# Optimization experiments

Hardware: AMD Instinct MI355X
Metric: run time of the kernel (lower is better)

The kernel has to match this reference:

```python
import jax, jax.numpy as jnp
import numpy as np
from jax import lax

B, T, C, H, W = 1, 6, 64, 128, 128
DG, K = 16, 9          # deformable groups, 3x3 kernel positions
CG = C // DG
MRM = 10.0             # max_residue_magnitude


def _conv3(x, w, b):
    y = lax.conv_general_dilated(x, w, (1, 1), 'SAME',
                                 dimension_numbers=('NCHW', 'OIHW', 'NCHW'))
    return y + b[None, :, None, None]


def _leaky(x):
    return jnp.where(x >= 0, x, 0.1 * x)


def _bilinear(img, py, px):
    # img [N,Cc,h,w]; py/px [N,*S] unnormalized pixel coords; zero padding outside.
    N, Cc, h, w = img.shape
    S = py.shape[1:]
    py = py.reshape(N, -1)
    px = px.reshape(N, -1)
    y0 = jnp.floor(py); x0 = jnp.floor(px)
    fy = py - y0; fx = px - x0
    y0 = y0.astype(jnp.int32); x0 = x0.astype(jnp.int32)
    imf = img.reshape(N, Cc, h * w)

    def corner(yi, xi, wt):
        valid = (yi >= 0) & (yi < h) & (xi >= 0) & (xi < w)
        idx = jnp.clip(yi, 0, h - 1) * w + jnp.clip(xi, 0, w - 1)
        v = jax.vmap(lambda im, ix: im[:, ix])(imf, idx)  # [N,Cc,M]
        return v * (wt * valid)[:, None, :]

    out = (corner(y0, x0, (1 - fy) * (1 - fx))
           + corner(y0, x0 + 1, (1 - fy) * fx)
           + corner(y0 + 1, x0, fy * (1 - fx))
           + corner(y0 + 1, x0 + 1, fy * fx))
    return out.reshape(N, Cc, *S)


def _flow_warp(x, flow):
    # flow [N,2,H,W]: channel 0 = x-displacement, channel 1 = y-displacement
    gy = jnp.arange(H, dtype=jnp.float32)
    gx = jnp.arange(W, dtype=jnp.float32)
    py = gy[None, :, None] + flow[:, 1]
    px = gx[None, None, :] + flow[:, 0]
    return _bilinear(x, py, px)


def _mod_deform_conv(x, offset, mask, w, b):
    # offset [N, 2*DG*K, H, W] interleaved (y,x) per (group, kernel pos); mask [N, DG*K, H, W]
    N = x.shape[0]
    off = offset.reshape(N, DG, K, 2, H, W)
    kh = (jnp.arange(K) // 3).astype(jnp.float32)
    kw = (jnp.arange(K) % 3).astype(jnp.float32)
    gy = jnp.arange(H, dtype=jnp.float32)
    gx = jnp.arange(W, dtype=jnp.float32)
    # stride 1, padding 1, dilation 1, 3x3 kernel
    py = gy[None, None, None, :, None] - 1.0 + kh[None, None, :, None, None] + off[:, :, :, 0]
    px = gx[None, None, None, None, :] - 1.0 + kw[None, None, :, None, None] + off[:, :, :, 1]
    xg = x.reshape(N, DG, CG, H, W).reshape(N * DG, CG, H, W)
    s = _bilinear(xg, py.reshape(N * DG, K, H, W), px.reshape(N * DG, K, H, W))
    s = s.reshape(N, DG, CG, K, H, W) * mask.reshape(N, DG, 1, K, H, W)
    wr = w.reshape(C, DG, CG, K)
    return jnp.einsum('ngckhw,ogck->nohw', s, wr) + b[None, :, None, None]


def setup_inputs() -> dict:
    key = jax.random.key(0)
    ks = jax.random.split(key, 10)
    rn = lambda k, s, sc: jax.random.normal(k, s, jnp.float32) * sc
    cin = 2 * C + 2  # (1 + n_frames//2)*C + n_frames
    return {
        'x': rn(ks[0], (B, T, C, H, W), 1.0),
        'flows_backward': rn(ks[1], (B, T - 1, 2, H, W), 2.0),
        'flows_forward': rn(ks[2], (B, T - 1, 2, H, W), 2.0),
        'cw1': rn(ks[3], (C, cin, 3, 3), 1.0 / np.sqrt(cin * 9)),
        'cb1': jnp.zeros((C,), jnp.float32),
        'cw2': rn(ks[4], (C, C, 3, 3), 1.0 / np.sqrt(C * 9)),
        'cb2': jnp.zeros((C,), jnp.float32),
        'cw3': rn(ks[5], (C, C, 3, 3), 1.0 / np.sqrt(C * 9)),
        'cb3': jnp.zeros((C,), jnp.float32),
        # original zero-inits the last conv; use small random so offsets/masks are nontrivial
        'cw4': rn(ks[6], (3 * K * DG, C, 3, 3), 0.01),
        'cb4': jnp.zeros((3 * K * DG,), jnp.float32),
        'dcn_w': rn(ks[7], (C, C, 3, 3), 1.0 / np.sqrt(C * 9)),
        'dcn_b': jnp.zeros((C,), jnp.float32),
    }


def reference(x, flows_backward, flows_forward, cw1, cb1, cw2, cb2, cw3, cb3,
              cw4, cb4, dcn_w, dcn_b):
    # Batch all backward-pass frame pairs (i=T-1..1) and forward-pass pairs (i=0..T-2)
    # into one effective batch of B*2*(T-1) independent DCN calls.
    xi = jnp.concatenate([x[:, 1:], x[:, :-1]], axis=1)      # source frames
    cur = jnp.concatenate([x[:, :-1], x[:, 1:]], axis=1)     # target (current) frames
    fl = jnp.concatenate([flows_backward, flows_forward], axis=1)
    N = B * 2 * (T - 1)
    xi = xi.reshape(N, C, H, W)
    cur = cur.reshape(N, C, H, W)
    fl = fl.reshape(N, 2, H, W)

    warped = _flow_warp(xi, fl)
    inp = jnp.concatenate([warped, cur, fl], axis=1)          # [N, 2C+2, H, W]
    h1 = _leaky(_conv3(inp, cw1, cb1))
    h2 = _leaky(_conv3(h1, cw2, cb2))
    h3 = _leaky(_conv3(h2, cw3, cb3))
    out = _conv3(h3, cw4, cb4)                                # [N, 3*9*DG, H, W]
    o1, o2, m = jnp.split(out, 3, axis=1)
    offset = MRM * jnp.tanh(jnp.concatenate([o1, o2], axis=1))
    # flow.flip(1).repeat -> interleaved (fy, fx) added to every (group, kernel pos)
    offset = offset + jnp.tile(fl[:, ::-1], (1, DG * K, 1, 1))
    mask = jax.nn.sigmoid(m)

    feat = _mod_deform_conv(xi, offset, mask, dcn_w, dcn_b)   # [N, C, H, W]
    feat = feat.reshape(B, 2, T - 1, C, H, W)
    zeros = jnp.zeros((B, 1, C, H, W), feat.dtype)
    x_backward = jnp.concatenate([feat[:, 0], zeros], axis=1)  # [B, T, C, H, W]
    x_forward = jnp.concatenate([zeros, feat[:, 1]], axis=1)   # [B, T, C, H, W]
    return x_backward, x_forward
```

## Files before the change

### kernel.cpp

```cpp
#include <hip/hip_runtime.h>
#include <math.h>

#define NP   10
#define C_   64
#define H_   128
#define W_   128
#define HW   (H_*W_)
#define MRM_ 10.0f

#define A_OFF   0u
#define SV_OFF  41472u
#define OMB_OFF 66048u
#define LDS_TOT 81408

#define W1T_N 82944
#define W2T_N 36864
#define W4_N  294912
#define DWT_N 49152

typedef __bf16 bf16x8 __attribute__((ext_vector_type(8)));
typedef float  f32x16 __attribute__((ext_vector_type(16)));

__device__ __forceinline__ f32x16 mfma32(bf16x8 a, bf16x8 b, f32x16 c) {
    return __builtin_amdgcn_mfma_f32_32x32x16_bf16(a, b, c, 0, 0, 0);
}

__device__ __forceinline__ ushort bfrn(float f) {
    uint u = __builtin_bit_cast(uint, f);
    u += 0x7FFFu + ((u >> 16) & 1u);
    return (ushort)(u >> 16);
}
__device__ __forceinline__ float blo(uint u) { return __builtin_bit_cast(float, u << 16); }
__device__ __forceinline__ float bhi(uint u) { return __builtin_bit_cast(float, u & 0xFFFF0000u); }
__device__ __forceinline__ float fast_tanh(float x) {
    float e = __expf(2.f * x);
    return 1.f - 2.f / (e + 1.f);
}

__device__ __forceinline__ const float* xi_base(const float* x, int n) {
    int f = (n < 5) ? (n + 1) : (n - 5);
    return x + (size_t)f * C_ * HW;
}
__device__ __forceinline__ const float* cur_base(const float* x, int n) {
    int f = (n < 5) ? n : (n - 4);
    return x + (size_t)f * C_ * HW;
}
__device__ __forceinline__ const float* fl_base(const float* fb, const float* ff, int n) {
    return (n < 5) ? (fb + (size_t)n * 2 * HW) : (ff + (size_t)(n - 5) * 2 * HW);
}

struct Bil { int i00, i01, i10, i11; float m00, m01, m10, m11; };
__device__ __forceinline__ Bil bil(float py, float px) {
    float y0f = floorf(py), x0f = floorf(px);
    int iy0 = (int)y0f, ix0 = (int)x0f;
    float ay = py - y0f, ax = px - x0f;
    bool v0y = (unsigned)iy0 < (unsigned)H_;
    bool v1y = (unsigned)(iy0 + 1) < (unsigned)H_;
    bool v0x = (unsigned)ix0 < (unsigned)W_;
    bool v1x = (unsigned)(ix0 + 1) < (unsigned)W_;
    int cy0 = min(max(iy0, 0), H_ - 1), cy1 = min(max(iy0 + 1, 0), H_ - 1);
    int cx0 = min(max(ix0, 0), W_ - 1), cx1 = min(max(ix0 + 1, 0), W_ - 1);
    Bil r;
    r.m00 = (1.f - ay) * (1.f - ax) * (float)(v0y && v0x);
    r.m01 = (1.f - ay) * ax         * (float)(v0y && v1x);
    r.m10 = ay * (1.f - ax)         * (float)(v1y && v0x);
    r.m11 = ay * ax                 * (float)(v1y && v1x);
    r.i00 = cy0 * W_ + cx0; r.i01 = cy0 * W_ + cx1;
    r.i10 = cy1 * W_ + cx0; r.i11 = cy1 * W_ + cx1;
    return r;
}

__global__ __launch_bounds__(256) void k_prep(
        const float* __restrict__ cw1, const float* __restrict__ cw2,
        const float* __restrict__ cw3, const float* __restrict__ cw4,
        const float* __restrict__ cb4, const float* __restrict__ dw,
        ushort* __restrict__ w1t, ushort* __restrict__ w2t,
        ushort* __restrict__ w3t, ushort* __restrict__ w4t,
        ushort* __restrict__ dwtb, float* __restrict__ pb4) {
    int id = blockIdx.x * 256 + threadIdx.x;
    if (id < W1T_N) {
        int blk = id >> 9, e = id & 511;
        int c = blk / 18, r = blk % 18; int t = r >> 1, nf = r & 1;
        int l = e >> 3, j = e & 7;
        int ci = c * 16 + (l >> 5) * 8 + j;
        int oc = nf * 32 + (l & 31);
        w1t[id] = (ci < 130) ? bfrn(cw1[((size_t)oc * 130 + ci) * 9 + t]) : (ushort)0;
        return;
    }
    id -= W1T_N;
    if (id < W2T_N) {
        int blk = id >> 9, e = id & 511;
        int c = blk / 18, r = blk % 18; int t = r >> 1, nf = r & 1;
        int l = e >> 3, j = e & 7;
        int ci = c * 16 + (l >> 5) * 8 + j;
        int oc = nf * 32 + (l & 31);
        w2t[id] = bfrn(cw2[((size_t)oc * 64 + ci) * 9 + t]);
        return;
    }
    id -= W2T_N;
    if (id < W2T_N) {
        int blk = id >> 9, e = id & 511;
        int c = blk / 18, r = blk % 18; int t = r >> 1, nf = r & 1;
        int l = e >> 3, j = e & 7;
        int ci = c * 16 + (l >> 5) * 8 + j;
        int oc = nf * 32 + (l & 31);
        w3t[id] = bfrn(cw3[((size_t)oc * 64 + ci) * 9 + t]);
        return;
    }
    id -= W2T_N;
    if (id < W4_N) {
        int blk = id >> 9, e = id & 511;
        int c = blk / 144, r = blk - c * 144;
        int t = r >> 4, g = r & 15;
        int l = e >> 3, j = e & 7;
        int nn = l & 31, kh = l >> 5;
        int ci = c * 16 + kh * 8 + j;
        int ch = (nn < 18) ? g * 18 + nn : (nn < 27 ? 288 + g * 9 + (nn - 18) : -1);
        float v = (ch >= 0) ? cw4[((size_t)ch * 64 + ci) * 9 + t] : 0.f;
        w4t[id] = bfrn(v);
        return;
    }
    id -= W4_N;
    if (id < DWT_N) {
        int blk = id >> 9, e = id & 511;
        int g = blk / 6, r = blk - g * 6;
        int kst = r >> 1, nf = r & 1;
        int l = e >> 3, j = e & 7;
        int kk = kst * 16 + (l >> 5) * 8 + j;
        int oc = nf * 32 + (l & 31);
        float v = (kk < 36) ? dw[((size_t)oc * 64 + g * 4 + (kk & 3)) * 9 + (kk >> 2)] : 0.f;
        dwtb[id] = bfrn(v);
        return;
    }
    id -= DWT_N;
    if (id < 512) {
        int g = id >> 5, nn = id & 31;
        int ch = (nn < 18) ? g * 18 + nn : (nn < 27 ? 288 + g * 9 + (nn - 18) : -1);
        pb4[id] = (ch >= 0) ? cb4[ch] : 0.f;
    }
}

__global__ __launch_bounds__(256) void k_warp(
        const float* __restrict__ x, const float* __restrict__ fb,
        const float* __restrict__ ff, ushort* __restrict__ warped) {
    int gid = blockIdx.x * 256 + threadIdx.x;
    int n = gid / HW, pos = gid % HW;
    int y = pos / W_, xx = pos % W_;
    const float* fl = fl_base(fb, ff, n);
    float fx = fl[pos], fy = fl[HW + pos];
    Bil b = bil((float)y + fy, (float)xx + fx);
    const float* xb = xi_base(x, n);
    ushort* wout = warped + (size_t)n * C_ * HW + pos;
    for (int c = 0; c < C_; ++c) {
        const float* p = xb + c * HW;
        wout[c * HW] = bfrn(b.m00 * p[b.i00] + b.m01 * p[b.i01]
                          + b.m10 * p[b.i10] + b.m11 * p[b.i11]);
    }
}

__global__ __launch_bounds__(256) void k_xt(
        const float* __restrict__ x, ushort* __restrict__ xt) {
    int gid = blockIdx.x * 256 + threadIdx.x;
    int f = gid / HW, pos = gid % HW;
    const float* src = x + (size_t)f * C_ * HW + pos;
    ushort* dst = xt + ((size_t)f * HW + pos) * 64;
    #pragma unroll
    for (int c8 = 0; c8 < 8; ++c8) {
        uint4 v;
        ushort h0 = bfrn(src[(c8 * 8 + 0) * HW]);
        ushort h1 = bfrn(src[(c8 * 8 + 1) * HW]);
        ushort h2 = bfrn(src[(c8 * 8 + 2) * HW]);
        ushort h3 = bfrn(src[(c8 * 8 + 3) * HW]);
        ushort h4 = bfrn(src[(c8 * 8 + 4) * HW]);
        ushort h5 = bfrn(src[(c8 * 8 + 5) * HW]);
        ushort h6 = bfrn(src[(c8 * 8 + 6) * HW]);
        ushort h7 = bfrn(src[(c8 * 8 + 7) * HW]);
        v.x = (uint)h0 | ((uint)h1 << 16);
        v.y = (uint)h2 | ((uint)h3 << 16);
        v.z = (uint)h4 | ((uint)h5 << 16);
        v.w = (uint)h6 | ((uint)h7 << 16);
        *(uint4*)(dst + c8 * 8) = v;
    }
}

template<int NCHUNK, int SRC>
__global__ __launch_bounds__(256, 3) void k_convm(
        const ushort* __restrict__ inb, const float* __restrict__ x,
        const float* __restrict__ fb, const float* __restrict__ ff,
        const ushort* __restrict__ wt, const float* __restrict__ bias,
        ushort* __restrict__ outp) {
    __shared__ __align__(16) char ldsb[41472];
    int tid = threadIdx.x;
    int lane = tid & 63, w = tid >> 6;
    int id = (blockIdx.x & 7) * 80 + (blockIdx.x >> 3);
    int bx = id & 7, by = (id >> 3) & 7, n = id >> 6;
    int col = lane & 31, khalf = lane >> 5;

    const float* flp = fl_base(fb, ff, n);
    const float* curp = cur_base(x, n);

    f32x16 acc[2][2];
    #pragma unroll
    for (int a = 0; a < 2; ++a)
        #pragma unroll
        for (int b = 0; b < 2; ++b)
            #pragma unroll
            for (int r = 0; r < 16; ++r) acc[a][b][r] = 0.f;

    int xb2 = col & 15;
    int rb0 = 4 * w + ((col >> 4) & 1);
    const int NPASS = (NCHUNK + 3) / 4;

    #pragma unroll
    for (int p = 0; p < NPASS; ++p) {
        const int c0 = 4 * p;
        const int cN = (NCHUNK - c0 >= 4) ? 4 : (NCHUNK - c0);
        __syncthreads();
        for (int cc = 0; cc < cN; ++cc) {
            int chunk = c0 + cc;
            int cbase = chunk * 16 + w * 4;
            for (int v = 0; v < 6; ++v) {
                int cell = v * 64 + lane;
                if (cell < 324) {
                    int cy = cell / 18, cx = cell - cy * 18;
                    int gy = by * 16 + cy - 1, gx = bx * 16 + cx - 1;
                    bool ok = ((unsigned)gy < 128u) && ((unsigned)gx < 128u);
                    int pos = gy * W_ + gx;
                    uint2 hv; hv.x = hv.y = 0;
                    if (SRC == 1 || chunk < 4) {
                        const ushort* sp = inb + ((size_t)n * 64 + cbase) * HW + pos;
                        ushort h0 = ok ? sp[0] : (ushort)0;
                        ushort h1 = ok ? sp[HW] : (ushort)0;
                        ushort h2 = ok ? sp[2 * HW] : (ushort)0;
                        ushort h3 = ok ? sp[3 * HW] : (ushort)0;
                        hv.x = (uint)h0 | ((uint)h1 << 16);
                        hv.y = (uint)h2 | ((uint)h3 << 16);
                    } else if (chunk < 8) {
                        const float* sp = curp + (size_t)(cbase - 64) * HW + pos;
                        ushort h0 = bfrn(ok ? sp[0] : 0.f);
                        ushort h1 = bfrn(ok ? sp[HW] : 0.f);
                        ushort h2 = bfrn(ok ? sp[2 * HW] : 0.f);
                        ushort h3 = bfrn(ok ? sp[3 * HW] : 0.f);
                        hv.x = (uint)h0 | ((uint)h1 << 16);
                        hv.y = (uint)h2 | ((uint)h3 << 16);
                    } else {
                        float v0 = 0.f, v1 = 0.f;
                        if (w == 0 && ok) { v0 = flp[pos]; v1 = flp[HW + pos]; }
                        hv.x = (uint)bfrn(v0) | ((uint)bfrn(v1) << 16);
                    }
                    uint byte = (uint)cell * 128 + (uint)cc * 32 + (uint)w * 8;
                    byte ^= ((uint)(cell & 7)) << 4;
                    *(uint2*)(ldsb + byte) = hv;
                }
            }
        }
        __syncthreads();
        for (int cc = 0; cc < cN; ++cc) {
            #pragma unroll
            for (int t = 0; t < 9; ++t) {
                const int ky = t / 3, kx = t % 3;
                size_t bb = (size_t)(((c0 + cc) * 9 + t) * 2) * 512 + (size_t)lane * 8;
                bf16x8 b0 = *(const bf16x8*)(wt + bb);
                bf16x8 b1 = *(const bf16x8*)(wt + bb + 512);
                #pragma unroll
                for (int f = 0; f < 2; ++f) {
                    int cell = (rb0 + 2 * f + ky) * 18 + xb2 + kx;
                    uint byte = (uint)cell * 128 + (uint)(2 * cc + khalf) * 16;
                    byte ^= ((uint)(cell & 7)) << 4;
                    bf16x8 a = *(const bf16x8*)(ldsb + byte);
                    acc[f][0] = mfma32(a, b0, acc[f][0]);
                    acc[f][1] = mfma32(a, b1, acc[f][1]);
                }
            }
        }
    }

    ushort* op = outp + (size_t)n * 64 * HW;
    #pragma unroll
    for (int f = 0; f < 2; ++f)
        #pragma unroll
        for (int nf = 0; nf < 2; ++nf) {
            int oc = nf * 32 + col;
            float bs = bias[oc];
            #pragma unroll
            for (int r = 0; r < 16; ++r) {
                int pxl = 64 * w + 32 * f + (r & 3) + 8 * (r >> 2) + 4 * khalf;
                int y = by * 16 + (pxl >> 4), xx = bx * 16 + (pxl & 15);
                float v = acc[f][nf][r] + bs;
                v = (v >= 0.f) ? v : 0.1f * v;
                op[(size_t)oc * HW + y * W_ + xx] = bfrn(v);
            }
        }
}

__global__ __launch_bounds__(256, 2) void k_dcn6(
        const ushort* __restrict__ h3, const ushort* __restrict__ xt,
        const float* __restrict__ fb, const float* __restrict__ ff,
        const ushort* __restrict__ w4hi,
        const ushort* __restrict__ dwtb, const float* __restrict__ pb4,
        const float* __restrict__ db, float* __restrict__ outb) {
    extern __shared__ __align__(16) char lds[];
    _Float16* OMBH = (_Float16*)(lds + OMB_OFF);

    int tid = threadIdx.x;
    int lane = tid & 63, w = tid >> 6;
    int id = (blockIdx.x & 7) * 80 + (blockIdx.x >> 3);
    int bx = id & 7, by = (id >> 3) & 7, n = id >> 6;
    int col = lane & 31, khalf = lane >> 5;

    const ushort* h3n = h3 + (size_t)n * 64 * HW;
    const float* fl = fl_base(fb, ff, n);
    int fxi = (n < 5) ? (n + 1) : (n - 5);
    const ushort* xtn = xt + (size_t)fxi * HW * 64;

    int Yp = by * 16 + (tid >> 4), Xp = bx * 16 + (tid & 15);
    float fxr = fl[Yp * W_ + Xp];
    float fyr = fl[HW + Yp * W_ + Xp];

    {
        uint pb = SV_OFF + (uint)tid * 96 + 72;
        *(unsigned long long*)(lds + pb)      = 0ull;
        *(unsigned long long*)(lds + pb + 8)  = 0ull;
        *(unsigned long long*)(lds + pb + 16) = 0ull;
    }

    for (int c = 0; c < 4; ++c) {
        for (int v = 0; v < 6; ++v) {
            int cell = v * 64 + lane;
            if (cell < 324) {
                int cy = cell / 18, cx = cell - cy * 18;
                int gy = by * 16 + cy - 1, gx = bx * 16 + cx - 1;
                bool ok = ((unsigned)gy < 128u) && ((unsigned)gx < 128u);
                const ushort* srcp = h3n + (size_t)(c * 16 + w * 4) * HW + gy * W_ + gx;
                ushort h0 = ok ? srcp[0] : (ushort)0;
                ushort h1 = ok ? srcp[HW] : (ushort)0;
                ushort h2 = ok ? srcp[2 * HW] : (ushort)0;
                ushort h3v = ok ? srcp[3 * HW] : (ushort)0;
                uint2 hv;
                hv.x = (uint)h0 | ((uint)h1 << 16);
                hv.y = (uint)h2 | ((uint)h3v << 16);
                uint byte = (uint)cell * 128 + (uint)c * 32 + (uint)w * 8;
                byte ^= ((uint)(cell & 7)) << 4;
                *(uint2*)(lds + byte) = hv;
            }
        }
    }
    __syncthreads();

    f32x16 zero16;
    #pragma unroll
    for (int r = 0; r < 16; ++r) zero16[r] = 0.f;

    f32x16 cd[2][2];
    #pragma unroll
    for (int a = 0; a < 2; ++a)
        #pragma unroll
        for (int b = 0; b < 2; ++b) cd[a][b] = zero16;

    int xb2 = col & 15;
    int rb0 = 4 * w + ((col >> 4) & 1);

    for (int sp = 0; sp < 8; ++sp) {
        int g0 = sp * 2;
        f32x16 c4[2][2];
        #pragma unroll
        for (int a = 0; a < 2; ++a)
            #pragma unroll
            for (int b = 0; b < 2; ++b) c4[a][b] = zero16;

        #pragma unroll 1
        for (int c = 0; c < 4; ++c) {
            #pragma unroll
            for (int t = 0; t < 9; ++t) {
                const int ky = t / 3, kx = t % 3;
                size_t bb = (size_t)((c * 9 + t) * 16) * 512 + (size_t)lane * 8;
                bf16x8 bh0 = *(const bf16x8*)(w4hi + bb + (size_t)g0 * 512);
                bf16x8 bh1 = *(const bf16x8*)(w4hi + bb + (size_t)(g0 + 1) * 512);
                #pragma unroll
                for (int f = 0; f < 2; ++f) {
                    int cell = (rb0 + 2 * f + ky) * 18 + xb2 + kx;
                    uint byte = (uint)cell * 128 + (uint)(2 * c + khalf) * 16;
                    byte ^= ((uint)(cell & 7)) << 4;
                    bf16x8 ah = *(const bf16x8*)(lds + byte);
                    c4[0][f] = mfma32(ah, bh0, c4[0][f]);
                    c4[1][f] = mfma32(ah, bh1, c4[1][f]);
                }
            }
        }

        #pragma unroll
        for (int gg = 0; gg < 2; ++gg) {
            int g = g0 + gg;
            __syncthreads();
            if (col < 27) {
                float pb = pb4[g * 32 + col];
                #pragma unroll
                for (int f = 0; f < 2; ++f)
                    #pragma unroll
                    for (int r = 0; r < 16; ++r) {
                        int pxl = 64 * w + 32 * f + (r & 3) + 8 * (r >> 2) + 4 * khalf;
                        float v = c4[gg][f][r] + pb;
                        v = (col < 18) ? MRM_ * fast_tanh(v) : 1.f / (1.f + __expf(-v));
                        OMBH[pxl * 30 + col] = (_Float16)v;
                    }
            }
            __syncthreads();
            {
                int px = tid;
                float Yf = (float)Yp, Xf = (float)Xp;
                const uint gof = (uint)g * 4;
                #pragma unroll
                for (int k = 0; k < 9; ++k) {
                    float oy = (float)OMBH[px * 30 + 2 * k] + fyr;
                    float ox = (float)OMBH[px * 30 + 2 * k + 1] + fxr;
                    float mk = (float)OMBH[px * 30 + 18 + k];
                    Bil b = bil(Yf - 1.f + (float)(k / 3) + oy,
                                Xf - 1.f + (float)(k % 3) + ox);
                    uint2 q00 = *(const uint2*)(xtn + (size_t)b.i00 * 64 + gof);
                    uint2 q01 = *(const uint2*)(xtn + (size_t)b.i01 * 64 + gof);
                    uint2 q10 = *(const uint2*)(xtn + (size_t)b.i10 * 64 + gof);
                    uint2 q11 = *(const uint2*)(xtn + (size_t)b.i11 * 64 + gof);
                    float s0 = b.m00 * blo(q00.x) + b.m01 * blo(q01.x)
                             + b.m10 * blo(q10.x) + b.m11 * blo(q11.x);
                    float s1 = b.m00 * bhi(q00.x) + b.m01 * bhi(q01.x)
                             + b.m10 * bhi(q10.x) + b.m11 * bhi(q11.x);
                    float s2 = b.m00 * blo(q00.y) + b.m01 * blo(q01.y)
                             + b.m10 * blo(q10.y) + b.m11 * blo(q11.y);
                    float s3 = b.m00 * bhi(q00.y) + b.m01 * bhi(q01.y)
                             + b.m10 * bhi(q10.y) + b.m11 * bhi(q11.y);
                    uint2 pk;
                    pk.x = (uint)bfrn(s0 * mk) | ((uint)bfrn(s1 * mk) << 16);
                    pk.y = (uint)bfrn(s2 * mk) | ((uint)bfrn(s3 * mk) << 16);
                    *(uint2*)(lds + (SV_OFF + (uint)px * 96 + (uint)k * 8)) = pk;
                }
            }
            __syncthreads();
            #pragma unroll
            for (int kst = 0; kst < 3; ++kst) {
                size_t dbb = (size_t)((g * 3 + kst) * 2) * 512 + (size_t)lane * 8;
                bf16x8 b0 = *(const bf16x8*)(dwtb + dbb);
                bf16x8 b1 = *(const bf16x8*)(dwtb + dbb + 512);
                #pragma unroll
                for (int f = 0; f < 2; ++f) {
                    int pxl = 64 * w + 32 * f + col;
                    uint byte = SV_OFF + (uint)pxl * 96 + (uint)(kst * 2 + khalf) * 16;
                    bf16x8 a = *(const bf16x8*)(lds + byte);
                    cd[f][0] = mfma32(a, b0, cd[f][0]);
                    cd[f][1] = mfma32(a, b1, cd[f][1]);
                }
            }
        }
    }

    float* base = (n < 5) ? outb + (size_t)n * 64 * HW
                          : outb + (size_t)(n + 2) * 64 * HW;
    #pragma unroll
    for (int f = 0; f < 2; ++f)
        #pragma unroll
        for (int nf = 0; nf < 2; ++nf) {
            int oc = nf * 32 + col;
            float bias = db[oc];
            #pragma unroll
            for (int r = 0; r < 16; ++r) {
                int pxl = 64 * w + 32 * f + (r & 3) + 8 * (r >> 2) + 4 * khalf;
                int y = by * 16 + (pxl >> 4), xx = bx * 16 + (pxl & 15);
                base[(size_t)oc * HW + y * W_ + xx] = cd[f][nf][r] + bias;
            }
        }
}

extern "C" void kernel_launch(void* const* d_in, const int* in_sizes, int n_in,
                              void* d_out, int out_size, void* d_ws, size_t ws_size,
                              hipStream_t stream) {
    (void)in_sizes; (void)n_in; (void)out_size; (void)ws_size;
    const float* x   = (const float*)d_in[0];
    const float* fb  = (const float*)d_in[1];
    const float* ff  = (const float*)d_in[2];
    const float* cw1 = (const float*)d_in[3];
    const float* cb1 = (const float*)d_in[4];
    const float* cw2 = (const float*)d_in[5];
    const float* cb2 = (const float*)d_in[6];
    const float* cw3 = (const float*)d_in[7];
    const float* cb3 = (const float*)d_in[8];
    const float* cw4 = (const float*)d_in[9];
    const float* cb4 = (const float*)d_in[10];
    const float* dw  = (const float*)d_in[11];
    const float* db  = (const float*)d_in[12];
    float* out = (float*)d_out;

    ushort* h1b  = (ushort*)d_ws;
    ushort* h3b  = h1b + 10485760;
    ushort* w1t  = h3b + 10485760;
    ushort* w2t  = w1t + W1T_N;
    ushort* w3t  = w2t + W2T_N;
    ushort* w4t  = w3t + W2T_N;
    ushort* dwtb = w4t + W4_N;
    float*  pb4  = (float*)(dwtb + DWT_N);
    ushort* xtb  = h1b;
    ushort* wpb  = (ushort*)d_out;
    ushort* h2b  = wpb + 10485760;

    (void)hipFuncSetAttribute((const void*)k_dcn6,
                              hipFuncAttributeMaxDynamicSharedMemorySize, LDS_TOT);

    k_prep<<<1958, 256, 0, stream>>>(cw1, cw2, cw3, cw4, cb4, dw,
                                     w1t, w2t, w3t, w4t, dwtb, pb4);
    k_warp<<<(NP * HW) / 256, 256, 0, stream>>>(x, fb, ff, wpb);
    k_convm<9, 0><<<640, 256, 0, stream>>>(wpb, x, fb, ff, w1t, cb1, h1b);
    k_convm<4, 1><<<640, 256, 0, stream>>>(h1b, x, fb, ff, w2t, cb2, h2b);
    k_xt<<<(6 * HW) / 256, 256, 0, stream>>>(x, xtb);
    k_convm<4, 1><<<640, 256, 0, stream>>>(h2b, x, fb, ff, w3t, cb3, h3b);

    hipMemsetAsync((char*)d_out + (size_t)5 * C_ * HW * sizeof(float), 0, (size_t)C_ * HW * sizeof(float), stream);
    hipMemsetAsync((char*)d_out + (size_t)6 * C_ * HW * sizeof(float), 0, (size_t)C_ * HW * sizeof(float), stream);

    k_dcn6<<<640, 256, LDS_TOT, stream>>>(h3b, xtb, fb, ff, w4t, dwtb, pb4, db, out);
}
```

Before: 716.4 us.

## Store DCN input group-planar for denser gathers and drop block barriers

The bf16 transposed input for the deformable conv changes layout. It was pixel-major with all 64 channels per pixel; it is now group-planar, one plane per deformable group holding 4 channels per pixel. Each bilinear gather for a group therefore touches 8-byte-strided neighbours instead of 128-byte-strided ones, which should improve cache-line use during the irregular sampling. The three __syncthreads in the per-group offset/mask and sampling phase become scheduling barriers, because each wave only writes and reads LDS rows for its own 64 pixels. This relies on that per-wave ownership staying exact; any cross-wave LDS dependency would become a race.

```diff
diff --git a/kernel.cpp b/kernel.cpp
--- a/kernel.cpp
+++ b/kernel.cpp
@@ -163,23 +163,17 @@
     int gid = blockIdx.x * 256 + threadIdx.x;
     int f = gid / HW, pos = gid % HW;
     const float* src = x + (size_t)f * C_ * HW + pos;
-    ushort* dst = xt + ((size_t)f * HW + pos) * 64;
-    #pragma unroll
-    for (int c8 = 0; c8 < 8; ++c8) {
-        uint4 v;
-        ushort h0 = bfrn(src[(c8 * 8 + 0) * HW]);
-        ushort h1 = bfrn(src[(c8 * 8 + 1) * HW]);
-        ushort h2 = bfrn(src[(c8 * 8 + 2) * HW]);
-        ushort h3 = bfrn(src[(c8 * 8 + 3) * HW]);
-        ushort h4 = bfrn(src[(c8 * 8 + 4) * HW]);
-        ushort h5 = bfrn(src[(c8 * 8 + 5) * HW]);
-        ushort h6 = bfrn(src[(c8 * 8 + 6) * HW]);
-        ushort h7 = bfrn(src[(c8 * 8 + 7) * HW]);
+    ushort* dst = xt + (size_t)f * 16 * HW * 4;
+    #pragma unroll
+    for (int g = 0; g < 16; ++g) {
+        uint2 v;
+        ushort h0 = bfrn(src[(g * 4 + 0) * HW]);
+        ushort h1 = bfrn(src[(g * 4 + 1) * HW]);
+        ushort h2 = bfrn(src[(g * 4 + 2) * HW]);
+        ushort h3 = bfrn(src[(g * 4 + 3) * HW]);
         v.x = (uint)h0 | ((uint)h1 << 16);
         v.y = (uint)h2 | ((uint)h3 << 16);
-        v.z = (uint)h4 | ((uint)h5 << 16);
-        v.w = (uint)h6 | ((uint)h7 << 16);
-        *(uint4*)(dst + c8 * 8) = v;
+        *(uint2*)(dst + ((size_t)g * HW + pos) * 4) = v;
     }
 }
 
@@ -293,7 +287,7 @@
         }
 }
 
-__global__ __launch_bounds__(256, 2) void k_dcn6(
+__global__ __launch_bounds__(256, 2) void k_dcn7(
         const ushort* __restrict__ h3, const ushort* __restrict__ xt,
         const float* __restrict__ fb, const float* __restrict__ ff,
         const ushort* __restrict__ w4hi,
@@ -311,7 +305,7 @@
     const ushort* h3n = h3 + (size_t)n * 64 * HW;
     const float* fl = fl_base(fb, ff, n);
     int fxi = (n < 5) ? (n + 1) : (n - 5);
-    const ushort* xtn = xt + (size_t)fxi * HW * 64;
+    const ushort* xtn = xt + (size_t)fxi * 16 * HW * 4;
 
     int Yp = by * 16 + (tid >> 4), Xp = bx * 16 + (tid & 15);
     float fxr = fl[Yp * W_ + Xp];
@@ -391,7 +385,7 @@
         #pragma unroll
         for (int gg = 0; gg < 2; ++gg) {
             int g = g0 + gg;
-            __syncthreads();
+            __builtin_amdgcn_sched_barrier(0);
             if (col < 27) {
                 float pb = pb4[g * 32 + col];
                 #pragma unroll
@@ -404,11 +398,11 @@
                         OMBH[pxl * 30 + col] = (_Float16)v;
                     }
             }
-            __syncthreads();
+            __builtin_amdgcn_sched_barrier(0);
             {
                 int px = tid;
                 float Yf = (float)Yp, Xf = (float)Xp;
-                const uint gof = (uint)g * 4;
+                const ushort* xg = xtn + (size_t)g * HW * 4;
                 #pragma unroll
                 for (int k = 0; k < 9; ++k) {
                     float oy = (float)OMBH[px * 30 + 2 * k] + fyr;
@@ -416,10 +410,10 @@
                     float mk = (float)OMBH[px * 30 + 18 + k];
                     Bil b = bil(Yf - 1.f + (float)(k / 3) + oy,
                                 Xf - 1.f + (float)(k % 3) + ox);
-                    uint2 q00 = *(const uint2*)(xtn + (size_t)b.i00 * 64 + gof);
-                    uint2 q01 = *(const uint2*)(xtn + (size_t)b.i01 * 64 + gof);
-                    uint2 q10 = *(const uint2*)(xtn + (size_t)b.i10 * 64 + gof);
-                    uint2 q11 = *(const uint2*)(xtn + (size_t)b.i11 * 64 + gof);
+                    uint2 q00 = *(const uint2*)(xg + (size_t)b.i00 * 4);
+                    uint2 q01 = *(const uint2*)(xg + (size_t)b.i01 * 4);
+                    uint2 q10 = *(const uint2*)(xg + (size_t)b.i10 * 4);
+                    uint2 q11 = *(const uint2*)(xg + (size_t)b.i11 * 4);
                     float s0 = b.m00 * blo(q00.x) + b.m01 * blo(q01.x)
                              + b.m10 * blo(q10.x) + b.m11 * blo(q11.x);
                     float s1 = b.m00 * bhi(q00.x) + b.m01 * bhi(q01.x)
@@ -434,7 +428,7 @@
                     *(uint2*)(lds + (SV_OFF + (uint)px * 96 + (uint)k * 8)) = pk;
                 }
             }
-            __syncthreads();
+            __builtin_amdgcn_sched_barrier(0);
             #pragma unroll
             for (int kst = 0; kst < 3; ++kst) {
                 size_t dbb = (size_t)((g * 3 + kst) * 2) * 512 + (size_t)lane * 8;
@@ -500,7 +494,7 @@
     ushort* wpb  = (ushort*)d_out;
     ushort* h2b  = wpb + 10485760;
 
-    (void)hipFuncSetAttribute((const void*)k_dcn6,
+    (void)hipFuncSetAttribute((const void*)k_dcn7,
                               hipFuncAttributeMaxDynamicSharedMemorySize, LDS_TOT);
 
     k_prep<<<1958, 256, 0, stream>>>(cw1, cw2, cw3, cw4, cb4, dw,
@@ -514,5 +508,5 @@
     hipMemsetAsync((char*)d_out + (size_t)5 * C_ * HW * sizeof(float), 0, (size_t)C_ * HW * sizeof(float), stream);
     hipMemsetAsync((char*)d_out + (size_t)6 * C_ * HW * sizeof(float), 0, (size_t)C_ * HW * sizeof(float), stream);
 
-    k_dcn6<<<640, 256, LDS_TOT, stream>>>(h3b, xtb, fb, ff, w4t, dwtb, pb4, db, out);
-}
+    k_dcn7<<<640, 256, LDS_TOT, stream>>>(h3b, xtb, fb, ff, w4t, dwtb, pb4, db, out);
+}
```

Measured after the change: 618.1 us. 1.16x faster.
